# Optimization experiments

Measured on AMD Instinct MI355X. Metric: run time of the kernel, lower is better.

Reference implementation:

```python
import jax, jax.numpy as jnp
import numpy as np

EPS = 1e-5

def setup_inputs() -> dict:
    key = jax.random.key(0)
    ks = jax.random.split(key, 10)
    B, C, H, W = 32, 512, 64, 64
    Cr = C // 16
    s = lambda n: 1.0 / np.sqrt(n)
    return {
        "x": jax.random.normal(ks[0], (B, C, H, W), jnp.float32),
        "w_mask": jax.random.normal(ks[1], (C,), jnp.float32) * s(C),   # conv_mask weight [1,C,1,1] -> [C]
        "b_mask": jax.random.normal(ks[2], (), jnp.float32) * 0.01,
        "w1": jax.random.normal(ks[3], (Cr, C), jnp.float32) * s(C),    # 1x1 conv C->Cr
        "b1": jax.random.normal(ks[4], (Cr,), jnp.float32) * 0.01,
        "ln_g": jnp.ones((Cr,), jnp.float32),
        "ln_b": jnp.zeros((Cr,), jnp.float32),
        "w2": jax.random.normal(ks[5], (C, Cr), jnp.float32) * s(Cr),   # 1x1 conv Cr->C
        "b2": jax.random.normal(ks[6], (C,), jnp.float32) * 0.01,
    }

def reference(x, w_mask, b_mask, w1, b1, ln_g, ln_b, w2, b2):
    B, C, H, W = x.shape
    xf = x.reshape(B, C, H * W)                                    # [B,C,HW]
    # spatial attention pooling (1x1 conv -> softmax over HW -> weighted sum)
    logits = jnp.einsum('bchw,c->bhw', x, w_mask).reshape(B, H * W) + b_mask
    attn = jax.nn.softmax(logits, axis=-1)                         # [B,HW]
    context = jnp.einsum('bcs,bs->bc', xf, attn)                   # [B,C]
    # bottleneck MLP gate: conv1 -> LayerNorm over Cr -> ReLU -> conv2 -> sigmoid
    t = context @ w1.T + b1                                        # [B,Cr]
    mu = jnp.mean(t, axis=-1, keepdims=True)
    var = jnp.mean(jnp.square(t - mu), axis=-1, keepdims=True)
    t = (t - mu) * jax.lax.rsqrt(var + EPS) * ln_g + ln_b
    t = jax.nn.relu(t)
    gate = jax.nn.sigmoid(t @ w2.T + b2)[:, :, None, None]         # [B,C,1,1]
    # instance norm (no affine, biased var over HW)
    m = jnp.mean(xf, axis=-1, keepdims=True)
    v = jnp.mean(jnp.square(xf - m), axis=-1, keepdims=True)
    xn = ((xf - m) * jax.lax.rsqrt(v + EPS)).reshape(B, C, H, W)
    return x * gate + (1.0 - gate) * xn
```

## Files before the change

### kernel.cpp

```cpp
#include <hip/hip_runtime.h>
#include <math.h>

#define B_   32
#define C_   512
#define CR_  32
#define HW_  4096
#define NCH  16
#define CPB  (C_/NCH)
#define EPSV 1e-5f

__global__ __launch_bounds__(256) void k1_logits_partial(
    const float* __restrict__ x, const float* __restrict__ w_mask,
    float* __restrict__ partial)
{
    const int b = blockIdx.y, ch = blockIdx.x, t = threadIdx.x;
    const int c0 = ch * CPB;
    float4 a0 = {0,0,0,0}, a1 = {0,0,0,0}, a2 = {0,0,0,0}, a3 = {0,0,0,0};
    for (int cc = 0; cc < CPB; ++cc) {
        const float w = w_mask[c0 + cc];
        const float4* px = reinterpret_cast<const float4*>(x + (size_t)(b * C_ + c0 + cc) * HW_);
        float4 v;
        v = px[t      ]; a0.x += w*v.x; a0.y += w*v.y; a0.z += w*v.z; a0.w += w*v.w;
        v = px[t + 256]; a1.x += w*v.x; a1.y += w*v.y; a1.z += w*v.z; a1.w += w*v.w;
        v = px[t + 512]; a2.x += w*v.x; a2.y += w*v.y; a2.z += w*v.z; a2.w += w*v.w;
        v = px[t + 768]; a3.x += w*v.x; a3.y += w*v.y; a3.z += w*v.z; a3.w += w*v.w;
    }
    float4* pp = reinterpret_cast<float4*>(partial + (size_t)(b * NCH + ch) * HW_);
    pp[t      ] = a0;
    pp[t + 256] = a1;
    pp[t + 512] = a2;
    pp[t + 768] = a3;
}

__global__ __launch_bounds__(256) void k2a_reduce(
    const float* __restrict__ partial, float* __restrict__ logits)
{
    const int b = blockIdx.y;
    const int i = blockIdx.x * 256 + threadIdx.x;
    float4 s = {0,0,0,0};
#pragma unroll
    for (int ch = 0; ch < NCH; ++ch) {
        const float4 v = reinterpret_cast<const float4*>(partial + (size_t)(b * NCH + ch) * HW_)[i];
        s.x += v.x; s.y += v.y; s.z += v.z; s.w += v.w;
    }
    reinterpret_cast<float4*>(logits + (size_t)b * HW_)[i] = s;
}

__global__ __launch_bounds__(256) void k2b_softmax(
    const float* __restrict__ logits, float* __restrict__ attn)
{
    __shared__ float l4[4];
    __shared__ float sM, sZ;
    const int b = blockIdx.x, t = threadIdx.x;
    const int lane = t & 63, wid = t >> 6;
    const float4* pl = reinterpret_cast<const float4*>(logits + (size_t)b * HW_);
    float4 v[4];
    float mx = -3.0e38f;
#pragma unroll
    for (int k = 0; k < 4; ++k) {
        v[k] = pl[t + 256 * k];
        mx = fmaxf(mx, fmaxf(fmaxf(v[k].x, v[k].y), fmaxf(v[k].z, v[k].w)));
    }
#pragma unroll
    for (int o = 32; o > 0; o >>= 1) mx = fmaxf(mx, __shfl_down(mx, o));
    if (lane == 0) l4[wid] = mx;
    __syncthreads();
    if (t == 0) sM = fmaxf(fmaxf(l4[0], l4[1]), fmaxf(l4[2], l4[3]));
    __syncthreads();
    const float M = sM;
    float e[16];
    float sum = 0.f;
#pragma unroll
    for (int k = 0; k < 4; ++k) {
        e[k*4+0] = expf(v[k].x - M);
        e[k*4+1] = expf(v[k].y - M);
        e[k*4+2] = expf(v[k].z - M);
        e[k*4+3] = expf(v[k].w - M);
        sum += e[k*4+0] + e[k*4+1] + e[k*4+2] + e[k*4+3];
    }
#pragma unroll
    for (int o = 32; o > 0; o >>= 1) sum += __shfl_down(sum, o);
    __syncthreads();
    if (lane == 0) l4[wid] = sum;
    __syncthreads();
    if (t == 0) sZ = l4[0] + l4[1] + l4[2] + l4[3];
    __syncthreads();
    const float rz = 1.f / sZ;
    float4* pa = reinterpret_cast<float4*>(attn + (size_t)b * HW_);
#pragma unroll
    for (int k = 0; k < 4; ++k)
        pa[t + 256 * k] = make_float4(e[k*4+0]*rz, e[k*4+1]*rz, e[k*4+2]*rz, e[k*4+3]*rz);
}

__global__ __launch_bounds__(256) void k3_context_stats(
    const float* __restrict__ x, const float* __restrict__ attn,
    float* __restrict__ ctx, float* __restrict__ sums, float* __restrict__ sqs)
{
    __shared__ float ld[12];
    const int b = blockIdx.y, c = blockIdx.x, t = threadIdx.x;
    const int lane = t & 63, wid = t >> 6;
    const float4* px = reinterpret_cast<const float4*>(x + (size_t)(b * C_ + c) * HW_);
    const float4* pa = reinterpret_cast<const float4*>(attn + (size_t)b * HW_);
    float dot = 0.f, sm = 0.f, sq = 0.f;
#pragma unroll
    for (int k = 0; k < 4; ++k) {
        const float4 xv = px[t + 256 * k];
        const float4 av = pa[t + 256 * k];
        dot += xv.x*av.x + xv.y*av.y + xv.z*av.z + xv.w*av.w;
        sm  += xv.x + xv.y + xv.z + xv.w;
        sq  += xv.x*xv.x + xv.y*xv.y + xv.z*xv.z + xv.w*xv.w;
    }
#pragma unroll
    for (int o = 32; o > 0; o >>= 1) {
        dot += __shfl_down(dot, o);
        sm  += __shfl_down(sm, o);
        sq  += __shfl_down(sq, o);
    }
    if (lane == 0) { ld[wid] = dot; ld[4 + wid] = sm; ld[8 + wid] = sq; }
    __syncthreads();
    if (t == 0) {
        ctx [b * C_ + c] = ld[0] + ld[1] + ld[2]  + ld[3];
        sums[b * C_ + c] = ld[4] + ld[5] + ld[6]  + ld[7];
        sqs [b * C_ + c] = ld[8] + ld[9] + ld[10] + ld[11];
    }
}

__global__ __launch_bounds__(256) void k4_mlp(
    const float* __restrict__ ctx, const float* __restrict__ w1, const float* __restrict__ b1,
    const float* __restrict__ ln_g, const float* __restrict__ ln_b,
    const float* __restrict__ w2, const float* __restrict__ b2,
    const float* __restrict__ sums, const float* __restrict__ sqs,
    float* __restrict__ Ab, float* __restrict__ Db)
{
    __shared__ float cs[C_];
    __shared__ float tl[CR_];
    const int b = blockIdx.x, t = threadIdx.x;
    cs[t]       = ctx[b * C_ + t];
    cs[t + 256] = ctx[b * C_ + t + 256];
    __syncthreads();

    const int row = t >> 3, sub = t & 7;
    float p = 0.f;
#pragma unroll 8
    for (int k = 0; k < 64; ++k) {
        const int c = sub + (k << 3);
        p += cs[c] * w1[row * C_ + c];
    }
    p += __shfl_down(p, 4, 8);
    p += __shfl_down(p, 2, 8);
    p += __shfl_down(p, 1, 8);
    if (sub == 0) tl[row] = p + b1[row];
    __syncthreads();

    float tn = 0.f;
    if (t < CR_) {
        float mu = 0.f;
#pragma unroll
        for (int i = 0; i < CR_; ++i) mu += tl[i];
        mu *= (1.f / CR_);
        float var = 0.f;
#pragma unroll
        for (int i = 0; i < CR_; ++i) { const float d = tl[i] - mu; var += d * d; }
        var *= (1.f / CR_);
        tn = (tl[t] - mu) * rsqrtf(var + EPSV) * ln_g[t] + ln_b[t];
        tn = fmaxf(tn, 0.f);
    }
    __syncthreads();
    if (t < CR_) tl[t] = tn;
    __syncthreads();

#pragma unroll
    for (int r = 0; r < 2; ++r) {
        const int c = t + r * 256;
        float g = b2[c];
#pragma unroll
        for (int i = 0; i < CR_; ++i) g += tl[i] * w2[c * CR_ + i];
        g = 1.f / (1.f + expf(-g));
        const float m  = sums[b * C_ + c] * (1.f / HW_);
        const float v  = sqs [b * C_ + c] * (1.f / HW_) - m * m;
        const float rn = rsqrtf(v + EPSV);
        Ab[b * C_ + c] = g + (1.f - g) * rn;
        Db[b * C_ + c] = -(1.f - g) * rn * m;
    }
}

__global__ __launch_bounds__(256) void k5_apply(
    const float* __restrict__ x, const float* __restrict__ Ab, const float* __restrict__ Db,
    float* __restrict__ out)
{
    const int b = blockIdx.y, c = blockIdx.x, t = threadIdx.x;
    const size_t base = (size_t)(b * C_ + c) * HW_;
    const float a = Ab[b * C_ + c], d = Db[b * C_ + c];
    const float4* px = reinterpret_cast<const float4*>(x + base);
    float4*       po = reinterpret_cast<float4*>(out + base);
#pragma unroll
    for (int k = 0; k < 4; ++k) {
        const float4 v = px[t + 256 * k];
        po[t + 256 * k] = make_float4(fmaf(a, v.x, d), fmaf(a, v.y, d),
                                      fmaf(a, v.z, d), fmaf(a, v.w, d));
    }
}

extern "C" void kernel_launch(void* const* d_in, const int* in_sizes, int n_in,
                              void* d_out, int out_size, void* d_ws, size_t ws_size,
                              hipStream_t stream)
{
    const float* x      = (const float*)d_in[0];
    const float* w_mask = (const float*)d_in[1];
    const float* w1     = (const float*)d_in[3];
    const float* b1     = (const float*)d_in[4];
    const float* ln_g   = (const float*)d_in[5];
    const float* ln_b   = (const float*)d_in[6];
    const float* w2     = (const float*)d_in[7];
    const float* b2     = (const float*)d_in[8];
    float* out = (float*)d_out;

    float* ws      = (float*)d_ws;
    float* partial = ws;
    float* logits  = partial + (size_t)B_ * NCH * HW_;
    float* attn    = logits + B_ * HW_;
    float* sums    = attn   + B_ * HW_;
    float* sqs     = sums   + B_ * C_;
    float* ctx     = sqs    + B_ * C_;
    float* Ab      = ctx    + B_ * C_;
    float* Db      = Ab     + B_ * C_;

    k1_logits_partial<<<dim3(NCH, B_), 256, 0, stream>>>(x, w_mask, partial);
    k2a_reduce<<<dim3(HW_ / 1024, B_), 256, 0, stream>>>(partial, logits);
    k2b_softmax<<<B_, 256, 0, stream>>>(logits, attn);
    k3_context_stats<<<dim3(C_, B_), 256, 0, stream>>>(x, attn, ctx, sums, sqs);
    k4_mlp<<<B_, 256, 0, stream>>>(ctx, w1, b1, ln_g, ln_b, w2, b2, sums, sqs, Ab, Db);
    k5_apply<<<dim3(C_, B_), 256, 0, stream>>>(x, Ab, Db, out);
}
```

Baseline: 199.1 us.

## Fuse partial-logit reduction into softmax, split k1 spatially, use nontemporal output stores

The separate k2a reduction kernel is folded into the softmax kernel, which now sums the 16 channel-chunk partials directly, removing one launch and the logits buffer round trip. The logits kernel gains a spatial grid dimension of two, doubling block count and halving per-thread accumulators to raise parallelism. The apply kernel writes its output with nontemporal stores to avoid polluting cache. The softmax now runs only 32 blocks that each read 16x more data, which could become a serial bottleneck.

Result: faster. 181.9 us (-8.6%).

```diff
diff --git a/kernel.cpp b/kernel.cpp
--- a/kernel.cpp
+++ b/kernel.cpp
@@ -9,58 +9,52 @@
 #define CPB  (C_/NCH)
 #define EPSV 1e-5f
 
+typedef float v4f __attribute__((ext_vector_type(4)));
+
 __global__ __launch_bounds__(256) void k1_logits_partial(
     const float* __restrict__ x, const float* __restrict__ w_mask,
     float* __restrict__ partial)
 {
     const int b = blockIdx.y, ch = blockIdx.x, t = threadIdx.x;
+    const int s0 = blockIdx.z * 512;
     const int c0 = ch * CPB;
-    float4 a0 = {0,0,0,0}, a1 = {0,0,0,0}, a2 = {0,0,0,0}, a3 = {0,0,0,0};
+    float4 a0 = {0,0,0,0}, a1 = {0,0,0,0};
+#pragma unroll 4
     for (int cc = 0; cc < CPB; ++cc) {
         const float w = w_mask[c0 + cc];
-        const float4* px = reinterpret_cast<const float4*>(x + (size_t)(b * C_ + c0 + cc) * HW_);
+        const float4* px = reinterpret_cast<const float4*>(x + (size_t)(b * C_ + c0 + cc) * HW_) + s0;
         float4 v;
         v = px[t      ]; a0.x += w*v.x; a0.y += w*v.y; a0.z += w*v.z; a0.w += w*v.w;
         v = px[t + 256]; a1.x += w*v.x; a1.y += w*v.y; a1.z += w*v.z; a1.w += w*v.w;
-        v = px[t + 512]; a2.x += w*v.x; a2.y += w*v.y; a2.z += w*v.z; a2.w += w*v.w;
-        v = px[t + 768]; a3.x += w*v.x; a3.y += w*v.y; a3.z += w*v.z; a3.w += w*v.w;
-    }
-    float4* pp = reinterpret_cast<float4*>(partial + (size_t)(b * NCH + ch) * HW_);
+    }
+    float4* pp = reinterpret_cast<float4*>(partial + (size_t)(b * NCH + ch) * HW_) + s0;
     pp[t      ] = a0;
     pp[t + 256] = a1;
-    pp[t + 512] = a2;
-    pp[t + 768] = a3;
-}
-
-__global__ __launch_bounds__(256) void k2a_reduce(
-    const float* __restrict__ partial, float* __restrict__ logits)
-{
-    const int b = blockIdx.y;
-    const int i = blockIdx.x * 256 + threadIdx.x;
-    float4 s = {0,0,0,0};
-#pragma unroll
-    for (int ch = 0; ch < NCH; ++ch) {
-        const float4 v = reinterpret_cast<const float4*>(partial + (size_t)(b * NCH + ch) * HW_)[i];
-        s.x += v.x; s.y += v.y; s.z += v.z; s.w += v.w;
-    }
-    reinterpret_cast<float4*>(logits + (size_t)b * HW_)[i] = s;
-}
-
-__global__ __launch_bounds__(256) void k2b_softmax(
-    const float* __restrict__ logits, float* __restrict__ attn)
+}
+
+__global__ __launch_bounds__(256) void k2_softmax(
+    const float* __restrict__ partial, float* __restrict__ attn)
 {
     __shared__ float l4[4];
     __shared__ float sM, sZ;
     const int b = blockIdx.x, t = threadIdx.x;
     const int lane = t & 63, wid = t >> 6;
-    const float4* pl = reinterpret_cast<const float4*>(logits + (size_t)b * HW_);
     float4 v[4];
+#pragma unroll
+    for (int k = 0; k < 4; ++k) {
+        float4 s = {0,0,0,0};
+        const int i = t + 256 * k;
+#pragma unroll
+        for (int ch = 0; ch < NCH; ++ch) {
+            const float4 p = reinterpret_cast<const float4*>(partial + (size_t)(b * NCH + ch) * HW_)[i];
+            s.x += p.x; s.y += p.y; s.z += p.z; s.w += p.w;
+        }
+        v[k] = s;
+    }
     float mx = -3.0e38f;
 #pragma unroll
-    for (int k = 0; k < 4; ++k) {
-        v[k] = pl[t + 256 * k];
+    for (int k = 0; k < 4; ++k)
         mx = fmaxf(mx, fmaxf(fmaxf(v[k].x, v[k].y), fmaxf(v[k].z, v[k].w)));
-    }
 #pragma unroll
     for (int o = 32; o > 0; o >>= 1) mx = fmaxf(mx, __shfl_down(mx, o));
     if (lane == 0) l4[wid] = mx;
@@ -192,12 +186,14 @@
     const size_t base = (size_t)(b * C_ + c) * HW_;
     const float a = Ab[b * C_ + c], d = Db[b * C_ + c];
     const float4* px = reinterpret_cast<const float4*>(x + base);
-    float4*       po = reinterpret_cast<float4*>(out + base);
+    v4f*          po = reinterpret_cast<v4f*>(out + base);
 #pragma unroll
     for (int k = 0; k < 4; ++k) {
         const float4 v = px[t + 256 * k];
-        po[t + 256 * k] = make_float4(fmaf(a, v.x, d), fmaf(a, v.y, d),
-                                      fmaf(a, v.z, d), fmaf(a, v.w, d));
+        v4f r;
+        r.x = fmaf(a, v.x, d); r.y = fmaf(a, v.y, d);
+        r.z = fmaf(a, v.z, d); r.w = fmaf(a, v.w, d);
+        __builtin_nontemporal_store(r, po + t + 256 * k);
     }
 }
 
@@ -217,17 +213,15 @@
 
     float* ws      = (float*)d_ws;
     float* partial = ws;
-    float* logits  = partial + (size_t)B_ * NCH * HW_;
-    float* attn    = logits + B_ * HW_;
+    float* attn    = partial + (size_t)B_ * NCH * HW_;
     float* sums    = attn   + B_ * HW_;
     float* sqs     = sums   + B_ * C_;
     float* ctx     = sqs    + B_ * C_;
     float* Ab      = ctx    + B_ * C_;
     float* Db      = Ab     + B_ * C_;
 
-    k1_logits_partial<<<dim3(NCH, B_), 256, 0, stream>>>(x, w_mask, partial);
-    k2a_reduce<<<dim3(HW_ / 1024, B_), 256, 0, stream>>>(partial, logits);
-    k2b_softmax<<<B_, 256, 0, stream>>>(logits, attn);
+    k1_logits_partial<<<dim3(NCH, B_, 2), 256, 0, stream>>>(x, w_mask, partial);
+    k2_softmax<<<B_, 256, 0, stream>>>(partial, attn);
     k3_context_stats<<<dim3(C_, B_), 256, 0, stream>>>(x, attn, ctx, sums, sqs);
     k4_mlp<<<B_, 256, 0, stream>>>(ctx, w1, b1, ln_g, ln_b, w2, b2, sums, sqs, Ab, Db);
     k5_apply<<<dim3(C_, B_), 256, 0, stream>>>(x, Ab, Db, out);
```
